# Optimization experiments

Measured on AMD Instinct MI355X. Metric: run time of the kernel, lower is better.

The kernel has to match this reference:

```python
import jax, jax.numpy as jnp
import numpy as np

B, T, K = 256, 1024, 128


def setup_inputs() -> dict:
    key = jax.random.key(0)
    k1, k2, k3, k4, k5 = jax.random.split(key, 5)
    emissions = jax.random.normal(k1, (B, T, K), dtype=jnp.float32)
    tags = jax.random.randint(k2, (B, T), 0, K)
    mask = jnp.ones((B, T), dtype=bool)
    # CRF parameters, init ~ uniform(-0.01, 0.01) as in the torch module
    transitions = jax.random.uniform(k3, (K, K), minval=-0.01, maxval=0.01, dtype=jnp.float32)
    start_transitions = jax.random.uniform(k4, (K,), minval=-0.01, maxval=0.01, dtype=jnp.float32)
    end_transitions = jax.random.uniform(k5, (K,), minval=-0.01, maxval=0.01, dtype=jnp.float32)
    return {"emissions": emissions, "transitions": transitions,
            "start_transitions": start_transitions, "end_transitions": end_transitions,
            "tags": tags, "mask": mask}


def _log_partition(emissions, transitions, start_transitions, end_transitions, mask):
    # emissions: [B,T,K], mask: [B,T] bool
    alpha0 = start_transitions[None, :] + emissions[:, 0, :]  # [B,K]

    def step(alpha, xs):
        emit_t, mask_t = xs  # [B,K], [B]
        scores = alpha[:, :, None] + transitions[None, :, :]  # [B,K,K]
        nxt = jax.nn.logsumexp(scores, axis=1) + emit_t       # [B,K]
        alpha = jnp.where(mask_t[:, None], nxt, alpha)
        return alpha, None

    emits = jnp.moveaxis(emissions[:, 1:, :], 1, 0)  # [T-1,B,K]
    masks = mask[:, 1:].T                            # [T-1,B]
    alpha, _ = jax.lax.scan(step, alpha0, (emits, masks))
    return jax.nn.logsumexp(alpha + end_transitions[None, :], axis=1)  # [B]


def _gold_score(emissions, transitions, start_transitions, end_transitions, tags, mask):
    maskf = mask.astype(emissions.dtype)
    first = tags[:, 0]
    score = start_transitions[first] + jnp.take_along_axis(emissions[:, 0, :], first[:, None], axis=1)[:, 0]
    trans_sc = transitions[tags[:, :-1], tags[:, 1:]]  # [B,T-1]
    emit_sc = jnp.take_along_axis(emissions[:, 1:, :], tags[:, 1:, None], axis=2)[..., 0]  # [B,T-1]
    score = score + jnp.sum((trans_sc + emit_sc) * maskf[:, 1:], axis=1)
    lengths = mask.astype(jnp.int32).sum(axis=1) - 1
    last_tags = jnp.take_along_axis(tags, lengths[:, None], axis=1)[:, 0]
    return score + end_transitions[last_tags]  # [B]


def reference(emissions, transitions, start_transitions, end_transitions, tags, mask):
    log_z = _log_partition(emissions, transitions, start_transitions, end_transitions, mask)
    gold = _gold_score(emissions, transitions, start_transitions, end_transitions, tags, mask)
    return log_z - gold  # per-sample negative log-likelihood, [B]
```

## Files before the change

kernel.cpp:

```cpp
#include <hip/hip_runtime.h>
#include <hip/hip_bf16.h>


typedef __attribute__((ext_vector_type(8))) short bf16x8;
typedef __attribute__((ext_vector_type(4))) float f32x4;

#define LOG2E 1.44269504088896340736f
#define LN2   0.69314718055994530942f

constexpr int K = 128, T = 1024, NB = 256;
constexpr int NGRP = 8;
constexpr int ROWS = 128;
constexpr float SCL = 8.0f;

__device__ inline unsigned short f2bf(float f) {
    unsigned u = __builtin_bit_cast(unsigned, f);
    u += 0x7FFFu + ((u >> 16) & 1u);
    return (unsigned short)(u >> 16);
}
__device__ inline unsigned packbf2(float x, float y) {
    return (unsigned)f2bf(x) | ((unsigned)f2bf(y) << 16);
}
__device__ inline unsigned cvtpk(float lo, float hi) {
    unsigned r;
    asm("v_cvt_pk_bf16_f32 %0, %1, %2" : "=v"(r) : "v"(lo), "v"(hi));
    return r;
}
__device__ inline float bflo(unsigned u) { return __builtin_bit_cast(float, u << 16); }
__device__ inline float bfhi(unsigned u) { return __builtin_bit_cast(float, u & 0xffff0000u); }
__device__ inline float fexp2(float x) { return __builtin_amdgcn_exp2f(x); }
__device__ inline float flog2(float x) { return __builtin_amdgcn_logf(x); }

__global__ void bpack_k(const float* __restrict__ tr, unsigned short* __restrict__ bp) {
    int idx = blockIdx.x * 256 + threadIdx.x;
    int l = idx & 63, ks = (idx >> 6) & 3, t = (idx >> 8) & 7, dir = idx >> 11;
    int c = l & 15, g = l >> 4;
    int n = 16 * t + c;
    unsigned w[4];
#pragma unroll
    for (int j = 0; j < 4; ++j) {
        int e0 = 2 * j, e1 = 2 * j + 1;
        int k0 = 16 * (2 * ks + (e0 >> 2)) + 4 * g + (e0 & 3);
        int k1 = 16 * (2 * ks + (e1 >> 2)) + 4 * g + (e1 & 3);
        float tv0 = dir ? tr[n * K + k0] : tr[k0 * K + n];
        float tv1 = dir ? tr[n * K + k1] : tr[k1 * K + n];
        w[j] = packbf2(fexp2(tv0 * LOG2E), fexp2(tv1 * LOG2E));
    }
    uint4 o; o.x = w[0]; o.y = w[1]; o.z = w[2]; o.w = w[3];
    *(uint4*)(bp + (size_t)idx * 8) = o;
}

__global__ __launch_bounds__(128, 2) void crf_seg(
    const float* __restrict__ em,
    const float* __restrict__ tr,
    const float* __restrict__ st,
    const float* __restrict__ en,
    const int*   __restrict__ tg,
    const unsigned short* __restrict__ bp,
    float* __restrict__ bnd_phi,
    float* __restrict__ bnd_psi,
    float* __restrict__ part)
{
    const int tid = threadIdx.x;
    const int wv = tid >> 6, l = tid & 63, c = l & 15, g = l >> 4;
    const int b = blockIdx.x >> 3, G = blockIdx.x & 7;

    __shared__ __align__(16) unsigned char eebuf[33024];
    __shared__ float shLse[16], shCr[16], shG[2];

    {
        const float* eb = em + ((size_t)b * T + (size_t)G * ROWS) * K;
        uint2* eev = (uint2*)eebuf;
#pragma unroll 16
        for (int it = 0; it < 32; ++it) {
            int flat = it * 128 + tid;
            int R = flat >> 5, q = flat & 31;
            float4 v = ((const float4*)eb)[flat];
            unsigned lo = cvtpk(fexp2(fmaf(v.x, LOG2E, -SCL)), fexp2(fmaf(v.y, LOG2E, -SCL)));
            unsigned hi = cvtpk(fexp2(fmaf(v.z, LOG2E, -SCL)), fexp2(fmaf(v.w, LOG2E, -SCL)));
            eev[R * 32 + (R >> 3) * 2 + q] = make_uint2(lo, hi);
        }
    }
    __syncthreads();

    bf16x8 Af[8][4];
    {
        const bf16x8* bpw = (const bf16x8*)bp;
#pragma unroll
        for (int t = 0; t < 8; ++t)
#pragma unroll
            for (int ks = 0; ks < 4; ++ks)
                Af[t][ks] = bpw[((wv * 8 + t) * 4 + ks) * 64 + l];
    }

    const uint2* eev = (const uint2*)eebuf;
    const int rbase = c * 258 + g;

    f32x4 acc[8];
#pragma unroll
    for (int t = 0; t < 8; ++t) { f32x4 o1 = {1.f, 1.f, 1.f, 1.f}; acc[t] = o1; }

#define BUILD_B()                                                      \
    bf16x8 B[4];                                                       \
    _Pragma("unroll")                                                  \
    for (int ks = 0; ks < 4; ++ks) {                                   \
        uint4 bu;                                                      \
        bu.x = cvtpk(acc[2 * ks][0], acc[2 * ks][1]);                  \
        bu.y = cvtpk(acc[2 * ks][2], acc[2 * ks][3]);                  \
        bu.z = cvtpk(acc[2 * ks + 1][0], acc[2 * ks + 1][1]);          \
        bu.w = cvtpk(acc[2 * ks + 1][2], acc[2 * ks + 1][3]);          \
        B[ks] = __builtin_bit_cast(bf16x8, bu);                        \
    }

#define DO_MFMA()                                                      \
    _Pragma("unroll")                                                  \
    for (int t = 0; t < 8; ++t) {                                      \
        f32x4 z = {0.f, 0.f, 0.f, 0.f};                                \
        z = __builtin_amdgcn_mfma_f32_16x16x32_bf16(Af[t][0], B[0], z, 0, 0, 0); \
        z = __builtin_amdgcn_mfma_f32_16x16x32_bf16(Af[t][1], B[1], z, 0, 0, 0); \
        z = __builtin_amdgcn_mfma_f32_16x16x32_bf16(Af[t][2], B[2], z, 0, 0, 0); \
        z = __builtin_amdgcn_mfma_f32_16x16x32_bf16(Af[t][3], B[3], z, 0, 0, 0); \
        acc[t] = z;                                                    \
    }

#define MUL_EE(EC)                                                     \
    _Pragma("unroll")                                                  \
    for (int t = 0; t < 8; ++t) {                                      \
        acc[t][0] *= bflo(EC[t].x);                                    \
        acc[t][1] *= bfhi(EC[t].x);                                    \
        acc[t][2] *= bflo(EC[t].y);                                    \
        acc[t][3] *= bfhi(EC[t].y);                                    \
    }

    if (wv == 0) {
        uint2 ecur[8];
#pragma unroll
        for (int i = 0; i < 8; ++i) {
#pragma unroll
            for (int t = 0; t < 8; ++t) ecur[t] = eev[rbase + i * 32 + 4 * t];
            BUILD_B()
            DO_MFMA()
            if (G == 0 && i == 0 && c == 0) {
#pragma unroll
                for (int t = 0; t < 8; ++t)
#pragma unroll
                    for (int r = 0; r < 4; ++r)
                        acc[t][r] = fexp2(st[16 * t + 4 * g + r] * LOG2E);
            }
            MUL_EE(ecur)
        }
    } else {
        uint2 ecur[8], enx[8];
#pragma unroll
        for (int t = 0; t < 8; ++t) ecur[t] = eev[rbase + 7 * 32 + 4 * t];
#pragma unroll
        for (int jj = 0; jj < 8; ++jj) {
            MUL_EE(ecur)
            if (jj < 7) {
#pragma unroll
                for (int t = 0; t < 8; ++t) enx[t] = eev[rbase + (6 - jj) * 32 + 4 * t];
            }
            BUILD_B()
            DO_MFMA()
#pragma unroll
            for (int t = 0; t < 8; ++t) ecur[t] = enx[t];
        }
    }
#undef BUILD_B
#undef DO_MFMA
#undef MUL_EE

    float gev, gtrv, genv;
    {
        const int t = G * ROWS + tid;
        int tgcur = tg[(size_t)b * T + t];
        int tgprev = __shfl_up(tgcur, 1);
        if (l == 0 && t > 0) tgprev = tg[(size_t)b * T + t - 1];
        gev  = em[((size_t)b * T + t) * K + tgcur];
        gtrv = (t == 0) ? st[tgcur] : tr[tgprev * K + tgcur];
        genv = (t == T - 1) ? en[tgcur] : 0.f;
    }

    __syncthreads();
    float* shF = (float*)eebuf;
    if (wv == 0) {
        float sum = 0.f;
#pragma unroll
        for (int t = 0; t < 8; ++t)
#pragma unroll
            for (int r = 0; r < 4; ++r) {
                shF[c * 132 + 16 * t + 4 * g + r] = acc[t][r];
                sum += acc[t][r];
            }
        sum += __shfl_xor(sum, 16);
        sum += __shfl_xor(sum, 32);
        if (g == 0) shLse[c] = flog2(sum) + 64.0f;
        if (c == 15) {
#pragma unroll
            for (int t = 0; t < 8; ++t)
#pragma unroll
                for (int r = 0; r < 4; ++r)
                    bnd_phi[((size_t)b * NGRP + G) * K + 16 * t + 4 * g + r] =
                        (flog2(acc[t][r]) + 64.f) * LN2;
        }
    } else if (c == 0) {
#pragma unroll
        for (int t = 0; t < 8; ++t)
#pragma unroll
            for (int r = 0; r < 4; ++r)
                bnd_psi[((size_t)b * NGRP + G) * K + 16 * t + 4 * g + r] =
                    (flog2(acc[t][r]) + 64.f) * LN2;
    }
    __syncthreads();
    if (wv == 1 && c >= 1) {
        float dot = 0.f;
#pragma unroll
        for (int t = 0; t < 8; ++t)
#pragma unroll
            for (int r = 0; r < 4; ++r)
                dot += acc[t][r] * shF[(c - 1) * 132 + 16 * t + 4 * g + r];
        dot += __shfl_xor(dot, 16);
        dot += __shfl_xor(dot, 32);
        if (g == 0) shCr[c] = (flog2(dot) + 128.f) - shLse[c];
    }
    {
        float gd = gtrv + gev + genv;
        gd += __shfl_xor(gd, 1);
        gd += __shfl_xor(gd, 2);
        gd += __shfl_xor(gd, 4);
        gd += __shfl_xor(gd, 8);
        gd += __shfl_xor(gd, 16);
        gd += __shfl_xor(gd, 32);
        if (l == 0) shG[wv] = gd;
    }
    __syncthreads();
    if (tid == 0) {
        float pt = 0.f;
#pragma unroll
        for (int cs = 1; cs < 16; ++cs) pt += shCr[cs];
        if (G > 0) pt -= shLse[0];
        part[b * NGRP + G] = pt * LN2 - (shG[0] + shG[1]);
    }
}

__device__ inline float waveLSE128(float a1, float a2) {
    float mx = fmaxf(a1, a2);
    mx = fmaxf(mx, __shfl_xor(mx, 1));
    mx = fmaxf(mx, __shfl_xor(mx, 2));
    mx = fmaxf(mx, __shfl_xor(mx, 4));
    mx = fmaxf(mx, __shfl_xor(mx, 8));
    mx = fmaxf(mx, __shfl_xor(mx, 16));
    mx = fmaxf(mx, __shfl_xor(mx, 32));
    float sm = fexp2((a1 - mx) * LOG2E) + fexp2((a2 - mx) * LOG2E);
    sm += __shfl_xor(sm, 1);
    sm += __shfl_xor(sm, 2);
    sm += __shfl_xor(sm, 4);
    sm += __shfl_xor(sm, 8);
    sm += __shfl_xor(sm, 16);
    sm += __shfl_xor(sm, 32);
    return mx + flog2(sm) * LN2;
}

__global__ __launch_bounds__(256, 1) void crf_fin(
    const float* __restrict__ en,
    const float* __restrict__ bnd_phi, const float* __restrict__ bnd_psi,
    const float* __restrict__ part, float* __restrict__ out)
{
    const int b = blockIdx.x, tid = threadIdx.x, l = tid & 63, wv = tid >> 6;
    __shared__ float redz[4];

    float z = 0.f;
    for (int tau = wv; tau < 8; tau += 4) {
        float a1, a2;
        if (tau < 7) {
            int Gx = tau + 1;
            a1 = bnd_psi[((size_t)b * NGRP + Gx) * K + l] +
                 bnd_phi[((size_t)b * NGRP + Gx - 1) * K + l];
            a2 = bnd_psi[((size_t)b * NGRP + Gx) * K + 64 + l] +
                 bnd_phi[((size_t)b * NGRP + Gx - 1) * K + 64 + l];
        } else {
            a1 = en[l]      + bnd_phi[((size_t)b * NGRP + 7) * K + l];
            a2 = en[64 + l] + bnd_phi[((size_t)b * NGRP + 7) * K + 64 + l];
        }
        z += waveLSE128(a1, a2);
    }
    if (l == 0) redz[wv] = z;
    __syncthreads();
    if (tid == 0) {
        float ps = 0.f;
#pragma unroll
        for (int Gx = 0; Gx < 8; ++Gx) ps += part[b * NGRP + Gx];
        out[b] = redz[0] + redz[1] + redz[2] + redz[3] + ps;
    }
}

extern "C" void kernel_launch(void* const* d_in, const int* in_sizes, int n_in,
                              void* d_out, int out_size, void* d_ws, size_t ws_size,
                              hipStream_t stream) {
    const float* em = (const float*)d_in[0];
    const float* tr = (const float*)d_in[1];
    const float* st = (const float*)d_in[2];
    const float* en = (const float*)d_in[3];
    const int*   tg = (const int*)d_in[4];

    unsigned short* bp = (unsigned short*)d_ws;
    float* bnd_phi = (float*)((char*)d_ws + 65536);
    float* bnd_psi = bnd_phi + (size_t)NB * NGRP * K;
    float* part    = bnd_psi + (size_t)NB * NGRP * K;
    float* out = (float*)d_out;

    bpack_k<<<16, 256, 0, stream>>>(tr, bp);
    crf_seg<<<NB * NGRP, 128, 0, stream>>>(em, tr, st, en, tg, bp, bnd_phi, bnd_psi, part);
    crf_fin<<<NB, 256, 0, stream>>>(en, bnd_phi, bnd_psi, part, out);
}
```

Measured before the change: 49.79 us.

## Swizzle LDS emission layout, split MFMA chains, hoist loads, set wave priority

Several changes land together in the segment kernel. The padded LDS layout is replaced by an XOR swizzle, so the buffer shrinks from 33024 to 32768 bytes. Matrix fragment loads and gold-score gathers are moved before the barrier so they overlap the emission staging. Each tile's four dependent MFMAs are split into two independent chains that are then summed, the first forward step uses a constant all-ones B operand, and MFMA sections are wrapped in s_setprio. These aim to cut LDS bank conflicts and MFMA dependency latency and to hide global load latency, at the cost of slightly higher register pressure and one extra vector add per tile.

Result: no change. 49.76 us (-0.1%).

```diff
diff --git a/kernel.cpp b/kernel.cpp
--- a/kernel.cpp
+++ b/kernel.cpp
@@ -65,8 +65,18 @@
     const int wv = tid >> 6, l = tid & 63, c = l & 15, g = l >> 4;
     const int b = blockIdx.x >> 3, G = blockIdx.x & 7;
 
-    __shared__ __align__(16) unsigned char eebuf[33024];
+    __shared__ __align__(16) unsigned char eebuf[32768];
     __shared__ float shLse[16], shCr[16], shG[2];
+
+    bf16x8 Af[8][4];
+    {
+        const bf16x8* bpw = (const bf16x8*)bp;
+#pragma unroll
+        for (int t = 0; t < 8; ++t)
+#pragma unroll
+            for (int ks = 0; ks < 4; ++ks)
+                Af[t][ks] = bpw[((wv * 8 + t) * 4 + ks) * 64 + l];
+    }
 
     {
         const float* eb = em + ((size_t)b * T + (size_t)G * ROWS) * K;
@@ -78,97 +88,9 @@
             float4 v = ((const float4*)eb)[flat];
             unsigned lo = cvtpk(fexp2(fmaf(v.x, LOG2E, -SCL)), fexp2(fmaf(v.y, LOG2E, -SCL)));
             unsigned hi = cvtpk(fexp2(fmaf(v.z, LOG2E, -SCL)), fexp2(fmaf(v.w, LOG2E, -SCL)));
-            eev[R * 32 + (R >> 3) * 2 + q] = make_uint2(lo, hi);
-        }
-    }
-    __syncthreads();
-
-    bf16x8 Af[8][4];
-    {
-        const bf16x8* bpw = (const bf16x8*)bp;
-#pragma unroll
-        for (int t = 0; t < 8; ++t)
-#pragma unroll
-            for (int ks = 0; ks < 4; ++ks)
-                Af[t][ks] = bpw[((wv * 8 + t) * 4 + ks) * 64 + l];
-    }
-
-    const uint2* eev = (const uint2*)eebuf;
-    const int rbase = c * 258 + g;
-
-    f32x4 acc[8];
-#pragma unroll
-    for (int t = 0; t < 8; ++t) { f32x4 o1 = {1.f, 1.f, 1.f, 1.f}; acc[t] = o1; }
-
-#define BUILD_B()                                                      \
-    bf16x8 B[4];                                                       \
-    _Pragma("unroll")                                                  \
-    for (int ks = 0; ks < 4; ++ks) {                                   \
-        uint4 bu;                                                      \
-        bu.x = cvtpk(acc[2 * ks][0], acc[2 * ks][1]);                  \
-        bu.y = cvtpk(acc[2 * ks][2], acc[2 * ks][3]);                  \
-        bu.z = cvtpk(acc[2 * ks + 1][0], acc[2 * ks + 1][1]);          \
-        bu.w = cvtpk(acc[2 * ks + 1][2], acc[2 * ks + 1][3]);          \
-        B[ks] = __builtin_bit_cast(bf16x8, bu);                        \
-    }
-
-#define DO_MFMA()                                                      \
-    _Pragma("unroll")                                                  \
-    for (int t = 0; t < 8; ++t) {                                      \
-        f32x4 z = {0.f, 0.f, 0.f, 0.f};                                \
-        z = __builtin_amdgcn_mfma_f32_16x16x32_bf16(Af[t][0], B[0], z, 0, 0, 0); \
-        z = __builtin_amdgcn_mfma_f32_16x16x32_bf16(Af[t][1], B[1], z, 0, 0, 0); \
-        z = __builtin_amdgcn_mfma_f32_16x16x32_bf16(Af[t][2], B[2], z, 0, 0, 0); \
-        z = __builtin_amdgcn_mfma_f32_16x16x32_bf16(Af[t][3], B[3], z, 0, 0, 0); \
-        acc[t] = z;                                                    \
-    }
-
-#define MUL_EE(EC)                                                     \
-    _Pragma("unroll")                                                  \
-    for (int t = 0; t < 8; ++t) {                                      \
-        acc[t][0] *= bflo(EC[t].x);                                    \
-        acc[t][1] *= bfhi(EC[t].x);                                    \
-        acc[t][2] *= bflo(EC[t].y);                                    \
-        acc[t][3] *= bfhi(EC[t].y);                                    \
-    }
-
-    if (wv == 0) {
-        uint2 ecur[8];
-#pragma unroll
-        for (int i = 0; i < 8; ++i) {
-#pragma unroll
-            for (int t = 0; t < 8; ++t) ecur[t] = eev[rbase + i * 32 + 4 * t];
-            BUILD_B()
-            DO_MFMA()
-            if (G == 0 && i == 0 && c == 0) {
-#pragma unroll
-                for (int t = 0; t < 8; ++t)
-#pragma unroll
-                    for (int r = 0; r < 4; ++r)
-                        acc[t][r] = fexp2(st[16 * t + 4 * g + r] * LOG2E);
-            }
-            MUL_EE(ecur)
-        }
-    } else {
-        uint2 ecur[8], enx[8];
-#pragma unroll
-        for (int t = 0; t < 8; ++t) ecur[t] = eev[rbase + 7 * 32 + 4 * t];
-#pragma unroll
-        for (int jj = 0; jj < 8; ++jj) {
-            MUL_EE(ecur)
-            if (jj < 7) {
-#pragma unroll
-                for (int t = 0; t < 8; ++t) enx[t] = eev[rbase + (6 - jj) * 32 + 4 * t];
-            }
-            BUILD_B()
-            DO_MFMA()
-#pragma unroll
-            for (int t = 0; t < 8; ++t) ecur[t] = enx[t];
-        }
-    }
-#undef BUILD_B
-#undef DO_MFMA
-#undef MUL_EE
+            eev[R * 32 + (q ^ ((R >> 3) << 1))] = make_uint2(lo, hi);
+        }
+    }
 
     float gev, gtrv, genv;
     {
@@ -180,49 +102,99 @@
         gtrv = (t == 0) ? st[tgcur] : tr[tgprev * K + tgcur];
         genv = (t == T - 1) ? en[tgcur] : 0.f;
     }
-
-    __syncthreads();
-    float* shF = (float*)eebuf;
+    __syncthreads();
+
+    const uint2* eev = (const uint2*)eebuf;
+    const int twoc = c << 1;
+
+    f32x4 acc[8];
+#pragma unroll
+    for (int t = 0; t < 8; ++t) { f32x4 o1 = {1.f, 1.f, 1.f, 1.f}; acc[t] = o1; }
+
+#define BUILD_B()                                                      \
+    _Pragma("unroll")                                                  \
+    for (int ks = 0; ks < 4; ++ks) {                                   \
+        uint4 bu;                                                      \
+        bu.x = cvtpk(acc[2 * ks][0], acc[2 * ks][1]);                  \
+        bu.y = cvtpk(acc[2 * ks][2], acc[2 * ks][3]);                  \
+        bu.z = cvtpk(acc[2 * ks + 1][0], acc[2 * ks + 1][1]);          \
+        bu.w = cvtpk(acc[2 * ks + 1][2], acc[2 * ks + 1][3]);          \
+        B[ks] = __builtin_bit_cast(bf16x8, bu);                        \
+    }
+
+#define DO_MFMA()                                                      \
+    __builtin_amdgcn_s_setprio(1);                                     \
+    _Pragma("unroll")                                                  \
+    for (int t = 0; t < 8; ++t) {                                      \
+        f32x4 z0 = {0.f, 0.f, 0.f, 0.f}, z1 = {0.f, 0.f, 0.f, 0.f};   \
+        z0 = __builtin_amdgcn_mfma_f32_16x16x32_bf16(Af[t][0], B[0], z0, 0, 0, 0); \
+        z0 = __builtin_amdgcn_mfma_f32_16x16x32_bf16(Af[t][1], B[1], z0, 0, 0, 0); \
+        z1 = __builtin_amdgcn_mfma_f32_16x16x32_bf16(Af[t][2], B[2], z1, 0, 0, 0); \
+        z1 = __builtin_amdgcn_mfma_f32_16x16x32_bf16(Af[t][3], B[3], z1, 0, 0, 0); \
+        acc[t] = z0 + z1;                                              \
+    }                                                                  \
+    __builtin_amdgcn_s_setprio(0);
+
+#define MUL_EE(EC)                                                     \
+    _Pragma("unroll")                                                  \
+    for (int t = 0; t < 8; ++t) {                                      \
+        f32x4 ev;                                                      \
+        ev[0] = bflo(EC[t].x); ev[1] = bfhi(EC[t].x);                  \
+        ev[2] = bflo(EC[t].y); ev[3] = bfhi(EC[t].y);                  \
+        acc[t] *= ev;                                                  \
+    }
+
     if (wv == 0) {
-        float sum = 0.f;
-#pragma unroll
-        for (int t = 0; t < 8; ++t)
-#pragma unroll
-            for (int r = 0; r < 4; ++r) {
-                shF[c * 132 + 16 * t + 4 * g + r] = acc[t][r];
-                sum += acc[t][r];
+        bf16x8 B[4];
+        uint2 ecur[8];
+#pragma unroll
+        for (int i = 0; i < 8; ++i) {
+            const int ro = (c * 8 + i) * 32;
+#pragma unroll
+            for (int t = 0; t < 8; ++t) ecur[t] = eev[ro + ((4 * t + g) ^ twoc)];
+            if (i == 0) {
+                uint4 bu; bu.x = bu.y = bu.z = bu.w = 0x3F803F80u;
+#pragma unroll
+                for (int ks = 0; ks < 4; ++ks) B[ks] = __builtin_bit_cast(bf16x8, bu);
+            } else {
+                BUILD_B()
             }
-        sum += __shfl_xor(sum, 16);
-        sum += __shfl_xor(sum, 32);
-        if (g == 0) shLse[c] = flog2(sum) + 64.0f;
-        if (c == 15) {
-#pragma unroll
-            for (int t = 0; t < 8; ++t)
-#pragma unroll
-                for (int r = 0; r < 4; ++r)
-                    bnd_phi[((size_t)b * NGRP + G) * K + 16 * t + 4 * g + r] =
-                        (flog2(acc[t][r]) + 64.f) * LN2;
-        }
-    } else if (c == 0) {
-#pragma unroll
-        for (int t = 0; t < 8; ++t)
-#pragma unroll
-            for (int r = 0; r < 4; ++r)
-                bnd_psi[((size_t)b * NGRP + G) * K + 16 * t + 4 * g + r] =
-                    (flog2(acc[t][r]) + 64.f) * LN2;
-    }
-    __syncthreads();
-    if (wv == 1 && c >= 1) {
-        float dot = 0.f;
-#pragma unroll
-        for (int t = 0; t < 8; ++t)
-#pragma unroll
-            for (int r = 0; r < 4; ++r)
-                dot += acc[t][r] * shF[(c - 1) * 132 + 16 * t + 4 * g + r];
-        dot += __shfl_xor(dot, 16);
-        dot += __shfl_xor(dot, 32);
-        if (g == 0) shCr[c] = (flog2(dot) + 128.f) - shLse[c];
-    }
+            DO_MFMA()
+            if (G == 0 && i == 0 && c == 0) {
+#pragma unroll
+                for (int t = 0; t < 8; ++t)
+#pragma unroll
+                    for (int r = 0; r < 4; ++r)
+                        acc[t][r] = fexp2(st[16 * t + 4 * g + r] * LOG2E);
+            }
+            MUL_EE(ecur)
+        }
+    } else {
+        bf16x8 B[4];
+        uint2 ecur[8], enx[8];
+        {
+            const int ro = (c * 8 + 7) * 32;
+#pragma unroll
+            for (int t = 0; t < 8; ++t) ecur[t] = eev[ro + ((4 * t + g) ^ twoc)];
+        }
+#pragma unroll
+        for (int jj = 0; jj < 8; ++jj) {
+            MUL_EE(ecur)
+            if (jj < 7) {
+                const int ro = (c * 8 + 6 - jj) * 32;
+#pragma unroll
+                for (int t = 0; t < 8; ++t) enx[t] = eev[ro + ((4 * t + g) ^ twoc)];
+            }
+            BUILD_B()
+            DO_MFMA()
+#pragma unroll
+            for (int t = 0; t < 8; ++t) ecur[t] = enx[t];
+        }
+    }
+#undef BUILD_B
+#undef DO_MFMA
+#undef MUL_EE
+
     {
         float gd = gtrv + gev + genv;
         gd += __shfl_xor(gd, 1);
@@ -232,6 +204,49 @@
         gd += __shfl_xor(gd, 16);
         gd += __shfl_xor(gd, 32);
         if (l == 0) shG[wv] = gd;
+    }
+
+    __syncthreads();
+    float* shF = (float*)eebuf;
+    if (wv == 0) {
+        float sum = 0.f;
+#pragma unroll
+        for (int t = 0; t < 8; ++t)
+#pragma unroll
+            for (int r = 0; r < 4; ++r) {
+                shF[c * 132 + 16 * t + 4 * g + r] = acc[t][r];
+                sum += acc[t][r];
+            }
+        sum += __shfl_xor(sum, 16);
+        sum += __shfl_xor(sum, 32);
+        if (g == 0) shLse[c] = flog2(sum) + 64.0f;
+        if (c == 15) {
+#pragma unroll
+            for (int t = 0; t < 8; ++t)
+#pragma unroll
+                for (int r = 0; r < 4; ++r)
+                    bnd_phi[((size_t)b * NGRP + G) * K + 16 * t + 4 * g + r] =
+                        (flog2(acc[t][r]) + 64.f) * LN2;
+        }
+    } else if (c == 0) {
+#pragma unroll
+        for (int t = 0; t < 8; ++t)
+#pragma unroll
+            for (int r = 0; r < 4; ++r)
+                bnd_psi[((size_t)b * NGRP + G) * K + 16 * t + 4 * g + r] =
+                    (flog2(acc[t][r]) + 64.f) * LN2;
+    }
+    __syncthreads();
+    if (wv == 1 && c >= 1) {
+        float dot = 0.f;
+#pragma unroll
+        for (int t = 0; t < 8; ++t)
+#pragma unroll
+            for (int r = 0; r < 4; ++r)
+                dot += acc[t][r] * shF[(c - 1) * 132 + 16 * t + 4 * g + r];
+        dot += __shfl_xor(dot, 16);
+        dot += __shfl_xor(dot, 32);
+        if (g == 0) shCr[c] = (flog2(dot) + 128.f) - shLse[c];
     }
     __syncthreads();
     if (tid == 0) {
```
